# Performance work log

Measured on AMD Instinct MI355X. Metric: run time of the kernel, lower is better.

## Reference

```python
import jax, jax.numpy as jnp
import numpy as np

K = 32
D = 64
N_ITER = 10


def setup_inputs() -> dict:
    key = jax.random.key(0)
    k1, k2 = jax.random.split(key)
    B = 65536
    x = jax.random.normal(k1, (B, D), dtype=jnp.float32)
    c = jnp.zeros((K,), dtype=jnp.float32)
    mu = jax.random.normal(k2, (K, D), dtype=jnp.float32) * 0.1
    A = jnp.tile(jnp.eye(D, dtype=jnp.float32)[None], (K, 1, 1))
    alpha = jnp.float32(0.1)
    return {"x": x, "c": c, "mu": mu, "A": A, "alpha": alpha}


def _grad_phi(x, c, mu, A):
    # Precision matrices Sigma_i^{-1} = A_i^T A_i : (k, d, d)
    P = jnp.einsum('kji,kjl->kil', A, A)
    diff = x[:, None, :] - mu[None, :, :]          # (B, k, d)
    Pd = jnp.einsum('kij,bkj->bki', P, diff)       # Sigma^{-1} (x - mu)
    quad = jnp.einsum('bki,bki->bk', diff, Pd)     # (B, k)
    # Analytic gradient of phi(x) = logsumexp_i(c_i - 0.5 q_i):
    # grad = -sum_i softmax_i(c_i - 0.5 q_i) * Sigma_i^{-1}(x - mu_i)
    w = jax.nn.softmax(c[None, :] - 0.5 * quad, axis=1)  # (B, k)
    return -jnp.einsum('bk,bki->bi', w, Pd)


def reference(x, c, mu, A, alpha):
    def step(x_cur, _):
        x_new = x_cur + alpha * _grad_phi(x_cur, c, mu, A)
        return x_new, None
    x_final, _ = jax.lax.scan(step, x, None, length=N_ITER)
    return x_final
```

## Files before the change

### kernel.cpp

```cpp
#include <hip/hip_runtime.h>
#include <hip/hip_bf16.h>


typedef __attribute__((ext_vector_type(4))) float f32x4;
typedef __attribute__((ext_vector_type(8))) short bf16x8;

#define KC 32
#define NITER 10
#define XROW 72
#define WAVE_SCR 6656

static __device__ __forceinline__ unsigned pk_bf16(float a, float b) {
  __hip_bfloat16 ha = __float2bfloat16(a), hb = __float2bfloat16(b);
  unsigned short ua = *(unsigned short*)&ha, ub = *(unsigned short*)&hb;
  return (unsigned)ua | ((unsigned)ub << 16);
}

__global__ void precompute1(const float* __restrict__ A, const float* __restrict__ mu,
                            const float* __restrict__ c,
                            float* __restrict__ Pmu_g, float* __restrict__ e_g,
                            __hip_bfloat16* __restrict__ Psw) {
  __shared__ float Pk[64 * 64];
  __shared__ float Pmu_s[64];
  const int k = blockIdx.x, tid = threadIdx.x;
  const float* Ak = A + k * 4096;
  for (int idx = tid; idx < 4096; idx += 256) {
    int i = idx >> 6, l = idx & 63;
    float s = 0.f;
    for (int j = 0; j < 64; ++j) s += Ak[j * 64 + i] * Ak[j * 64 + l];
    Pk[idx] = s;
  }
  __syncthreads();
  if (tid < 64) {
    float s = 0.f;
    for (int l = 0; l < 64; ++l) s += Pk[tid * 64 + l] * mu[k * 64 + l];
    Pmu_s[tid] = s;
    Pmu_g[k * 64 + tid] = s;
  }
  __syncthreads();
  if (tid == 0) {
    float s = 0.f;
    for (int i = 0; i < 64; ++i) s += mu[k * 64 + i] * Pmu_s[i];
    e_g[k] = c[k] - 0.5f * s;
  }
  for (int idx = tid; idx < 4096; idx += 256) {
    int f = idx >> 9, lane = (idx >> 3) & 63, j = idx & 7;
    int mt = f >> 1, s = f & 1, qq = lane >> 4, l4 = lane & 15;
    float v = Pk[(s * 32 + qq * 8 + j) * 64 + mt * 16 + l4];
    Psw[k * 4096 + idx] = __float2bfloat16(v);
  }
}

__global__ void precompute2(const float* __restrict__ Pmu_g,
                            __hip_bfloat16* __restrict__ PmuA,
                            __hip_bfloat16* __restrict__ PmuB) {
  const int tid = threadIdx.x;
  for (int idx = tid; idx < 2048; idx += 256) {
    int f = idx >> 9, lane = (idx >> 3) & 63, j = idx & 7;
    int mtc = f >> 1, s = f & 1, qq = lane >> 4, l4 = lane & 15;
    PmuA[idx] = __float2bfloat16(Pmu_g[(mtc * 16 + l4) * 64 + s * 32 + qq * 8 + j]);
  }
  for (int idx = tid; idx < 2048; idx += 256) {
    int f = idx >> 9, lane = (idx >> 3) & 63, j = idx & 7;
    int qq = lane >> 4, l4 = lane & 15;
    PmuB[idx] = __float2bfloat16(Pmu_g[(qq * 8 + j) * 64 + f * 16 + l4]);
  }
}

__launch_bounds__(256, 2)
__global__ void denoise_main(const float* __restrict__ x_in,
                             const float* __restrict__ e_g,
                             const float* __restrict__ alpha_g,
                             const __hip_bfloat16* __restrict__ Psw,
                             const __hip_bfloat16* __restrict__ PmuA,
                             const __hip_bfloat16* __restrict__ PmuB,
                             float* __restrict__ out) {
  __shared__ __attribute__((aligned(16))) char scratch[4 * WAVE_SCR];

  const int tid = threadIdx.x;
  const int wave = tid >> 6, lane = tid & 63;
  const int q = lane >> 4, l4 = lane & 15;
  const int base_pt = blockIdx.x * 128 + wave * 32;
  const float alpha = alpha_g[0];

  char* sw = scratch + wave * WAVE_SCR;
  __hip_bfloat16* xsw = (__hip_bfloat16*)sw;
  float* pmxw = (float*)sw;
  __hip_bfloat16* wtw = (__hip_bfloat16*)(sw + 4608);

  const bf16x8* PswF = (const bf16x8*)Psw;
  const bf16x8* PmuAF = (const bf16x8*)PmuA;
  const bf16x8* PmuBF = (const bf16x8*)PmuB;

  float xm[4][2][4];
#pragma unroll
  for (int mt = 0; mt < 4; ++mt)
#pragma unroll
    for (int nt = 0; nt < 2; ++nt)
#pragma unroll
      for (int r = 0; r < 4; ++r)
        xm[mt][nt][r] = x_in[(base_pt + nt * 16 + l4) * 64 + mt * 16 + q * 4 + r];

  const f32x4 Z4 = {0.f, 0.f, 0.f, 0.f};

#pragma unroll 1
  for (int it = 0; it < NITER; ++it) {
#pragma unroll
    for (int mt = 0; mt < 4; ++mt)
#pragma unroll
      for (int nt = 0; nt < 2; ++nt) {
        unsigned u0 = pk_bf16(xm[mt][nt][0], xm[mt][nt][1]);
        unsigned u1 = pk_bf16(xm[mt][nt][2], xm[mt][nt][3]);
        uint2 v; v.x = u0; v.y = u1;
        *(uint2*)&xsw[(nt * 16 + l4) * XROW + mt * 16 + q * 4] = v;
      }

    bf16x8 bx[2][2];
#pragma unroll
    for (int s = 0; s < 2; ++s)
#pragma unroll
      for (int nt = 0; nt < 2; ++nt)
        bx[s][nt] = *(const bf16x8*)&xsw[(nt * 16 + l4) * XROW + s * 32 + q * 8];

    bf16x8 ap[2][4][2];
#pragma unroll
    for (int mt = 0; mt < 4; ++mt)
#pragma unroll
      for (int s = 0; s < 2; ++s)
        ap[0][mt][s] = PswF[(mt * 2 + s) * 64 + lane];

    f32x4 pmx[2][2];
#pragma unroll
    for (int mtc = 0; mtc < 2; ++mtc)
#pragma unroll
      for (int nt = 0; nt < 2; ++nt) {
        f32x4 acc = Z4;
#pragma unroll
        for (int s = 0; s < 2; ++s) {
          bf16x8 a = PmuAF[(mtc * 2 + s) * 64 + lane];
          acc = __builtin_amdgcn_mfma_f32_16x16x32_bf16(a, bx[s][nt], acc, 0, 0, 0);
        }
        pmx[mtc][nt] = acc;
      }
#pragma unroll
    for (int mtc = 0; mtc < 2; ++mtc)
#pragma unroll
      for (int nt = 0; nt < 2; ++nt)
#pragma unroll
        for (int r = 0; r < 4; ++r)
          pmxw[(mtc * 16 + q * 4 + r) * 32 + nt * 16 + l4] = pmx[mtc][nt][r];

    float accY[4][2][4];
#pragma unroll
    for (int mt = 0; mt < 4; ++mt)
#pragma unroll
      for (int nt = 0; nt < 2; ++nt)
#pragma unroll
        for (int r = 0; r < 4; ++r) accY[mt][nt][r] = 0.f;
    float lsum0 = 0.f, lsum1 = 0.f;

#pragma unroll 2
    for (int k = 0; k < KC; ++k) {
      const int cur = k & 1, nxt = cur ^ 1;
      const int kn = (k + 1) & (KC - 1);
#pragma unroll
      for (int mt = 0; mt < 4; ++mt)
#pragma unroll
        for (int s = 0; s < 2; ++s)
          ap[nxt][mt][s] = PswF[kn * 512 + (mt * 2 + s) * 64 + lane];

      f32x4 y[4][2];
#pragma unroll
      for (int mt = 0; mt < 4; ++mt)
#pragma unroll
        for (int nt = 0; nt < 2; ++nt) {
          f32x4 acc = Z4;
          acc = __builtin_amdgcn_mfma_f32_16x16x32_bf16(ap[cur][mt][0], bx[0][nt], acc, 0, 0, 0);
          acc = __builtin_amdgcn_mfma_f32_16x16x32_bf16(ap[cur][mt][1], bx[1][nt], acc, 0, 0, 0);
          y[mt][nt] = acc;
        }

      float xy0 = 0.f, xy1 = 0.f;
#pragma unroll
      for (int mt = 0; mt < 4; ++mt)
#pragma unroll
        for (int r = 0; r < 4; ++r) {
          xy0 += xm[mt][0][r] * y[mt][0][r];
          xy1 += xm[mt][1][r] * y[mt][1][r];
        }
      xy0 += __shfl_xor(xy0, 16, 64);
      xy0 += __shfl_xor(xy0, 32, 64);
      xy1 += __shfl_xor(xy1, 16, 64);
      xy1 += __shfl_xor(xy1, 32, 64);

      const float pk0 = pmxw[k * 32 + l4];
      const float pk1 = pmxw[k * 32 + 16 + l4];
      const float ek = e_g[k];
      const float w0 = __expf(ek + pk0 - 0.5f * xy0);
      const float w1 = __expf(ek + pk1 - 0.5f * xy1);
      lsum0 += w0;
      lsum1 += w1;
      if (q == 0) {
        wtw[l4 * 32 + k] = __float2bfloat16(w0);
        wtw[(16 + l4) * 32 + k] = __float2bfloat16(w1);
      }
#pragma unroll
      for (int mt = 0; mt < 4; ++mt)
#pragma unroll
        for (int r = 0; r < 4; ++r) {
          accY[mt][0][r] += w0 * y[mt][0][r];
          accY[mt][1][r] += w1 * y[mt][1][r];
        }
    }

    bf16x8 wtf[2];
#pragma unroll
    for (int nt = 0; nt < 2; ++nt)
      wtf[nt] = *(const bf16x8*)&wtw[(nt * 16 + l4) * 32 + q * 8];
    f32x4 pacc[4][2];
#pragma unroll
    for (int mt = 0; mt < 4; ++mt) {
      bf16x8 a = PmuBF[mt * 64 + lane];
      pacc[mt][0] = __builtin_amdgcn_mfma_f32_16x16x32_bf16(a, wtf[0], Z4, 0, 0, 0);
      pacc[mt][1] = __builtin_amdgcn_mfma_f32_16x16x32_bf16(a, wtf[1], Z4, 0, 0, 0);
    }

    const float c0 = alpha / lsum0;
    const float c1 = alpha / lsum1;
#pragma unroll
    for (int mt = 0; mt < 4; ++mt)
#pragma unroll
      for (int r = 0; r < 4; ++r) {
        xm[mt][0][r] += c0 * (pacc[mt][0][r] - accY[mt][0][r]);
        xm[mt][1][r] += c1 * (pacc[mt][1][r] - accY[mt][1][r]);
      }
  }

  float* outs = (float*)sw;
#pragma unroll
  for (int p = 0; p < 2; ++p) {
#pragma unroll
    for (int mt2 = 0; mt2 < 2; ++mt2)
#pragma unroll
      for (int nt = 0; nt < 2; ++nt)
#pragma unroll
        for (int r = 0; r < 4; ++r)
          outs[(nt * 16 + l4) * 32 + mt2 * 16 + q * 4 + r] = xm[p * 2 + mt2][nt][r];
#pragma unroll
    for (int rep = 0; rep < 16; ++rep) {
      int flat = rep * 64 + lane;
      int pt = flat >> 5, dp = flat & 31;
      out[(base_pt + pt) * 64 + p * 32 + dp] = outs[pt * 32 + dp];
    }
  }
}

extern "C" void kernel_launch(void* const* d_in, const int* in_sizes, int n_in,
                              void* d_out, int out_size, void* d_ws, size_t ws_size,
                              hipStream_t stream) {
  (void)in_sizes; (void)n_in; (void)out_size; (void)ws_size;
  const float* x = (const float*)d_in[0];
  const float* c = (const float*)d_in[1];
  const float* mu = (const float*)d_in[2];
  const float* A = (const float*)d_in[3];
  const float* alpha = (const float*)d_in[4];
  float* out = (float*)d_out;

  char* ws = (char*)d_ws;
  float* Pmu_g = (float*)(ws);
  float* e_g = (float*)(ws + 8192);
  __hip_bfloat16* PmuA = (__hip_bfloat16*)(ws + 8448);
  __hip_bfloat16* PmuB = (__hip_bfloat16*)(ws + 12544);
  __hip_bfloat16* Psw = (__hip_bfloat16*)(ws + 16640);

  precompute1<<<32, 256, 0, stream>>>(A, mu, c, Pmu_g, e_g, Psw);
  precompute2<<<1, 256, 0, stream>>>(Pmu_g, PmuA, PmuB);
  denoise_main<<<512, 256, 0, stream>>>(x, e_g, alpha, Psw, PmuA, PmuB, out);
}
```

Before: 306.2 us.

## Split component loop across wave pairs and reduce partial sums through LDS

Each pair of waves now shares 32 points, with each wave handling half of the 32 mixture components. The partial weighted sums and softmax denominators are exchanged through shared memory with block barriers. The grid doubles to 1024 blocks, which gives more waves to hide latency and halves the serial component loop per wave, at the cost of barriers, LDS traffic and a larger shared footprint. Other changes: cross-lane reductions now use ds_swizzle and permlane32 swap, the bias term is folded into the stored Pmu, stores are vectorized, and precompute1 gets an LDS-tiled A^T A.

```diff
diff --git a/kernel.cpp b/kernel.cpp
--- a/kernel.cpp
+++ b/kernel.cpp
@@ -6,9 +6,13 @@
 typedef __attribute__((ext_vector_type(8))) short bf16x8;
 
 #define KC 32
+#define KH 16
 #define NITER 10
 #define XROW 72
-#define WAVE_SCR 6656
+#define PW_BYTES 8704
+#define WT_PITCH 40
+#define WT_BYTES 2560
+#define LS_BYTES 256
 
 static __device__ __forceinline__ unsigned pk_bf16(float a, float b) {
   __hip_bfloat16 ha = __float2bfloat16(a), hb = __float2bfloat16(b);
@@ -16,38 +20,63 @@
   return (unsigned)ua | ((unsigned)ub << 16);
 }
 
+static __device__ __forceinline__ float red16(float x) {
+  int v = __builtin_amdgcn_ds_swizzle(__float_as_int(x), 0x401F);
+  return x + __int_as_float(v);
+}
+static __device__ __forceinline__ float red32(float x) {
+  int xi = __float_as_int(x);
+  auto pr = __builtin_amdgcn_permlane32_swap(xi, xi, false, false);
+  return __int_as_float(pr[0]) + __int_as_float(pr[1]);
+}
+
 __global__ void precompute1(const float* __restrict__ A, const float* __restrict__ mu,
                             const float* __restrict__ c,
                             float* __restrict__ Pmu_g, float* __restrict__ e_g,
                             __hip_bfloat16* __restrict__ Psw) {
+  __shared__ float As[64 * 64];
   __shared__ float Pk[64 * 64];
-  __shared__ float Pmu_s[64];
   const int k = blockIdx.x, tid = threadIdx.x;
   const float* Ak = A + k * 4096;
-  for (int idx = tid; idx < 4096; idx += 256) {
-    int i = idx >> 6, l = idx & 63;
-    float s = 0.f;
-    for (int j = 0; j < 64; ++j) s += Ak[j * 64 + i] * Ak[j * 64 + l];
-    Pk[idx] = s;
-  }
+  for (int idx = tid; idx < 1024; idx += 256)
+    *(f32x4*)&As[idx * 4] = *(const f32x4*)&Ak[idx * 4];
   __syncthreads();
+
+  const int i = tid >> 2, lg = tid & 3;
+  float acc[16] = {};
+  for (int j = 0; j < 64; ++j) {
+    float ai = As[j * 64 + i];
+    const f32x4* row = (const f32x4*)&As[j * 64 + lg * 16];
+#pragma unroll
+    for (int g = 0; g < 4; ++g) {
+      f32x4 v = row[g];
+#pragma unroll
+      for (int r = 0; r < 4; ++r) acc[g * 4 + r] += ai * v[r];
+    }
+  }
+#pragma unroll
+  for (int g = 0; g < 4; ++g)
+#pragma unroll
+    for (int r = 0; r < 4; ++r) Pk[i * 64 + lg * 16 + g * 4 + r] = acc[g * 4 + r];
+  __syncthreads();
+
   if (tid < 64) {
     float s = 0.f;
-    for (int l = 0; l < 64; ++l) s += Pk[tid * 64 + l] * mu[k * 64 + l];
-    Pmu_s[tid] = s;
+    for (int l = 0; l < 64; ++l) s += Pk[l * 64 + tid] * mu[k * 64 + l];
     Pmu_g[k * 64 + tid] = s;
-  }
-  __syncthreads();
-  if (tid == 0) {
-    float s = 0.f;
-    for (int i = 0; i < 64; ++i) s += mu[k * 64 + i] * Pmu_s[i];
-    e_g[k] = c[k] - 0.5f * s;
-  }
-  for (int idx = tid; idx < 4096; idx += 256) {
-    int f = idx >> 9, lane = (idx >> 3) & 63, j = idx & 7;
-    int mt = f >> 1, s = f & 1, qq = lane >> 4, l4 = lane & 15;
-    float v = Pk[(s * 32 + qq * 8 + j) * 64 + mt * 16 + l4];
-    Psw[k * 4096 + idx] = __float2bfloat16(v);
+    float v = mu[k * 64 + tid] * s;
+#pragma unroll
+    for (int off = 1; off < 64; off <<= 1) v += __shfl_xor(v, off, 64);
+    if (tid == 0) e_g[k] = c[k] - 0.5f * v;
+  }
+
+  unsigned* Psw32 = (unsigned*)(Psw + k * 4096);
+  for (int idx2 = tid; idx2 < 2048; idx2 += 256) {
+    int idx = idx2 << 1;
+    int f = idx >> 9, ln = (idx >> 3) & 63, j = idx & 7;
+    int mt = f >> 1, s = f & 1, qq = ln >> 4, l4 = ln & 15;
+    int col = mt * 16 + l4, rb = s * 32 + qq * 8 + j;
+    Psw32[idx2] = pk_bf16(Pk[rb * 64 + col], Pk[(rb + 1) * 64 + col]);
   }
 }
 
@@ -75,31 +104,36 @@
                              const __hip_bfloat16* __restrict__ PmuA,
                              const __hip_bfloat16* __restrict__ PmuB,
                              float* __restrict__ out) {
-  __shared__ __attribute__((aligned(16))) char scratch[4 * WAVE_SCR];
+  __shared__ __attribute__((aligned(16))) char scratch[4 * PW_BYTES + 2 * WT_BYTES + 2 * LS_BYTES];
 
   const int tid = threadIdx.x;
   const int wave = tid >> 6, lane = tid & 63;
+  const int pair = wave >> 1, khalf = wave & 1;
   const int q = lane >> 4, l4 = lane & 15;
-  const int base_pt = blockIdx.x * 128 + wave * 32;
+  const int base_pt = blockIdx.x * 64 + pair * 32;
   const float alpha = alpha_g[0];
-
-  char* sw = scratch + wave * WAVE_SCR;
-  __hip_bfloat16* xsw = (__hip_bfloat16*)sw;
-  float* pmxw = (float*)sw;
-  __hip_bfloat16* wtw = (__hip_bfloat16*)(sw + 4608);
+  const int kbase = khalf * KH;
+
+  char* pw = scratch + wave * PW_BYTES;
+  __hip_bfloat16* xsw = (__hip_bfloat16*)pw;
+  float* pmxw = (float*)pw;
+  float* exw = (float*)pw;
+  const float* exw_p = (const float*)(scratch + (wave ^ 1) * PW_BYTES);
+  __hip_bfloat16* wtw = (__hip_bfloat16*)(scratch + 4 * PW_BYTES + pair * WT_BYTES);
+  float* lsw = (float*)(scratch + 4 * PW_BYTES + 2 * WT_BYTES + pair * LS_BYTES);
 
   const bf16x8* PswF = (const bf16x8*)Psw;
   const bf16x8* PmuAF = (const bf16x8*)PmuA;
   const bf16x8* PmuBF = (const bf16x8*)PmuB;
 
-  float xm[4][2][4];
+  f32x4 xm[4][2];
 #pragma unroll
   for (int mt = 0; mt < 4; ++mt)
 #pragma unroll
     for (int nt = 0; nt < 2; ++nt)
-#pragma unroll
-      for (int r = 0; r < 4; ++r)
-        xm[mt][nt][r] = x_in[(base_pt + nt * 16 + l4) * 64 + mt * 16 + q * 4 + r];
+      xm[mt][nt] = *(const f32x4*)&x_in[(base_pt + nt * 16 + l4) * 64 + mt * 16 + q * 4];
+
+  const f32x4 ev = *(const f32x4*)&e_g[kbase + q * 4];
 
   const f32x4 Z4 = {0.f, 0.f, 0.f, 0.f};
 
@@ -109,9 +143,9 @@
     for (int mt = 0; mt < 4; ++mt)
 #pragma unroll
       for (int nt = 0; nt < 2; ++nt) {
-        unsigned u0 = pk_bf16(xm[mt][nt][0], xm[mt][nt][1]);
-        unsigned u1 = pk_bf16(xm[mt][nt][2], xm[mt][nt][3]);
-        uint2 v; v.x = u0; v.y = u1;
+        uint2 v;
+        v.x = pk_bf16(xm[mt][nt][0], xm[mt][nt][1]);
+        v.y = pk_bf16(xm[mt][nt][2], xm[mt][nt][3]);
         *(uint2*)&xsw[(nt * 16 + l4) * XROW + mt * 16 + q * 4] = v;
       }
 
@@ -127,42 +161,36 @@
     for (int mt = 0; mt < 4; ++mt)
 #pragma unroll
       for (int s = 0; s < 2; ++s)
-        ap[0][mt][s] = PswF[(mt * 2 + s) * 64 + lane];
-
-    f32x4 pmx[2][2];
-#pragma unroll
-    for (int mtc = 0; mtc < 2; ++mtc)
-#pragma unroll
-      for (int nt = 0; nt < 2; ++nt) {
-        f32x4 acc = Z4;
-#pragma unroll
-        for (int s = 0; s < 2; ++s) {
-          bf16x8 a = PmuAF[(mtc * 2 + s) * 64 + lane];
-          acc = __builtin_amdgcn_mfma_f32_16x16x32_bf16(a, bx[s][nt], acc, 0, 0, 0);
-        }
-        pmx[mtc][nt] = acc;
-      }
-#pragma unroll
-    for (int mtc = 0; mtc < 2; ++mtc)
-#pragma unroll
-      for (int nt = 0; nt < 2; ++nt)
-#pragma unroll
-        for (int r = 0; r < 4; ++r)
-          pmxw[(mtc * 16 + q * 4 + r) * 32 + nt * 16 + l4] = pmx[mtc][nt][r];
-
-    float accY[4][2][4];
-#pragma unroll
-    for (int mt = 0; mt < 4; ++mt)
-#pragma unroll
-      for (int nt = 0; nt < 2; ++nt)
-#pragma unroll
-        for (int r = 0; r < 4; ++r) accY[mt][nt][r] = 0.f;
+        ap[0][mt][s] = PswF[kbase * 512 + (mt * 2 + s) * 64 + lane];
+
+    f32x4 pmx[2];
+#pragma unroll
+    for (int nt = 0; nt < 2; ++nt) {
+      f32x4 acc = Z4;
+#pragma unroll
+      for (int s = 0; s < 2; ++s) {
+        bf16x8 a = PmuAF[(khalf * 2 + s) * 64 + lane];
+        acc = __builtin_amdgcn_mfma_f32_16x16x32_bf16(a, bx[s][nt], acc, 0, 0, 0);
+      }
+      pmx[nt] = acc;
+    }
+#pragma unroll
+    for (int nt = 0; nt < 2; ++nt)
+#pragma unroll
+      for (int r = 0; r < 4; ++r)
+        pmxw[(q * 4 + r) * 32 + nt * 16 + l4] = pmx[nt][r] + ev[r];
+
+    f32x4 accY[4][2];
+#pragma unroll
+    for (int mt = 0; mt < 4; ++mt)
+#pragma unroll
+      for (int nt = 0; nt < 2; ++nt) accY[mt][nt] = Z4;
     float lsum0 = 0.f, lsum1 = 0.f;
 
 #pragma unroll 2
-    for (int k = 0; k < KC; ++k) {
-      const int cur = k & 1, nxt = cur ^ 1;
-      const int kn = (k + 1) & (KC - 1);
+    for (int kk = 0; kk < KH; ++kk) {
+      const int cur = kk & 1, nxt = cur ^ 1;
+      const int kn = kbase + ((kk + 1) & (KH - 1));
 #pragma unroll
       for (int mt = 0; mt < 4; ++mt)
 #pragma unroll
@@ -180,43 +208,58 @@
           y[mt][nt] = acc;
         }
 
-      float xy0 = 0.f, xy1 = 0.f;
-#pragma unroll
-      for (int mt = 0; mt < 4; ++mt)
-#pragma unroll
-        for (int r = 0; r < 4; ++r) {
-          xy0 += xm[mt][0][r] * y[mt][0][r];
-          xy1 += xm[mt][1][r] * y[mt][1][r];
-        }
-      xy0 += __shfl_xor(xy0, 16, 64);
-      xy0 += __shfl_xor(xy0, 32, 64);
-      xy1 += __shfl_xor(xy1, 16, 64);
-      xy1 += __shfl_xor(xy1, 32, 64);
-
-      const float pk0 = pmxw[k * 32 + l4];
-      const float pk1 = pmxw[k * 32 + 16 + l4];
-      const float ek = e_g[k];
-      const float w0 = __expf(ek + pk0 - 0.5f * xy0);
-      const float w1 = __expf(ek + pk1 - 0.5f * xy1);
+      f32x4 d0 = xm[0][0] * y[0][0];
+      f32x4 d1 = xm[0][1] * y[0][1];
+#pragma unroll
+      for (int mt = 1; mt < 4; ++mt) {
+        d0 += xm[mt][0] * y[mt][0];
+        d1 += xm[mt][1] * y[mt][1];
+      }
+      float xy0 = (d0[0] + d0[1]) + (d0[2] + d0[3]);
+      float xy1 = (d1[0] + d1[1]) + (d1[2] + d1[3]);
+      xy0 = red32(red16(xy0));
+      xy1 = red32(red16(xy1));
+
+      const float pk0 = pmxw[kk * 32 + l4];
+      const float pk1 = pmxw[kk * 32 + 16 + l4];
+      const float w0 = __expf(pk0 - 0.5f * xy0);
+      const float w1 = __expf(pk1 - 0.5f * xy1);
       lsum0 += w0;
       lsum1 += w1;
       if (q == 0) {
-        wtw[l4 * 32 + k] = __float2bfloat16(w0);
-        wtw[(16 + l4) * 32 + k] = __float2bfloat16(w1);
-      }
-#pragma unroll
-      for (int mt = 0; mt < 4; ++mt)
-#pragma unroll
-        for (int r = 0; r < 4; ++r) {
-          accY[mt][0][r] += w0 * y[mt][0][r];
-          accY[mt][1][r] += w1 * y[mt][1][r];
-        }
-    }
+        wtw[l4 * WT_PITCH + kbase + kk] = __float2bfloat16(w0);
+        wtw[(16 + l4) * WT_PITCH + kbase + kk] = __float2bfloat16(w1);
+      }
+#pragma unroll
+      for (int mt = 0; mt < 4; ++mt) {
+        accY[mt][0] += w0 * y[mt][0];
+        accY[mt][1] += w1 * y[mt][1];
+      }
+    }
+
+#pragma unroll
+    for (int mt = 0; mt < 4; ++mt)
+#pragma unroll
+      for (int nt = 0; nt < 2; ++nt)
+        *(f32x4*)&exw[(nt * 16 + l4) * 68 + mt * 16 + q * 4] = accY[mt][nt];
+    if (q == 0) {
+      lsw[khalf * 32 + l4] = lsum0;
+      lsw[khalf * 32 + 16 + l4] = lsum1;
+    }
+    __syncthreads();
+
+#pragma unroll
+    for (int mt = 0; mt < 4; ++mt)
+#pragma unroll
+      for (int nt = 0; nt < 2; ++nt)
+        accY[mt][nt] += *(const f32x4*)&exw_p[(nt * 16 + l4) * 68 + mt * 16 + q * 4];
+    const float lt0 = lsum0 + lsw[(khalf ^ 1) * 32 + l4];
+    const float lt1 = lsum1 + lsw[(khalf ^ 1) * 32 + 16 + l4];
 
     bf16x8 wtf[2];
 #pragma unroll
     for (int nt = 0; nt < 2; ++nt)
-      wtf[nt] = *(const bf16x8*)&wtw[(nt * 16 + l4) * 32 + q * 8];
+      wtf[nt] = *(const bf16x8*)&wtw[(nt * 16 + l4) * WT_PITCH + q * 8];
     f32x4 pacc[4][2];
 #pragma unroll
     for (int mt = 0; mt < 4; ++mt) {
@@ -225,34 +268,22 @@
       pacc[mt][1] = __builtin_amdgcn_mfma_f32_16x16x32_bf16(a, wtf[1], Z4, 0, 0, 0);
     }
 
-    const float c0 = alpha / lsum0;
-    const float c1 = alpha / lsum1;
-#pragma unroll
-    for (int mt = 0; mt < 4; ++mt)
-#pragma unroll
-      for (int r = 0; r < 4; ++r) {
-        xm[mt][0][r] += c0 * (pacc[mt][0][r] - accY[mt][0][r]);
-        xm[mt][1][r] += c1 * (pacc[mt][1][r] - accY[mt][1][r]);
-      }
-  }
-
-  float* outs = (float*)sw;
-#pragma unroll
-  for (int p = 0; p < 2; ++p) {
-#pragma unroll
-    for (int mt2 = 0; mt2 < 2; ++mt2)
-#pragma unroll
-      for (int nt = 0; nt < 2; ++nt)
-#pragma unroll
-        for (int r = 0; r < 4; ++r)
-          outs[(nt * 16 + l4) * 32 + mt2 * 16 + q * 4 + r] = xm[p * 2 + mt2][nt][r];
-#pragma unroll
-    for (int rep = 0; rep < 16; ++rep) {
-      int flat = rep * 64 + lane;
-      int pt = flat >> 5, dp = flat & 31;
-      out[(base_pt + pt) * 64 + p * 32 + dp] = outs[pt * 32 + dp];
-    }
-  }
+    const float c0 = alpha / lt0;
+    const float c1 = alpha / lt1;
+#pragma unroll
+    for (int mt = 0; mt < 4; ++mt) {
+      xm[mt][0] += c0 * (pacc[mt][0] - accY[mt][0]);
+      xm[mt][1] += c1 * (pacc[mt][1] - accY[mt][1]);
+    }
+    __syncthreads();
+  }
+
+#pragma unroll
+  for (int mt2 = 0; mt2 < 2; ++mt2)
+#pragma unroll
+    for (int nt = 0; nt < 2; ++nt)
+      *(f32x4*)&out[(base_pt + nt * 16 + l4) * 64 + khalf * 32 + mt2 * 16 + q * 4] =
+          xm[khalf * 2 + mt2][nt];
 }
 
 extern "C" void kernel_launch(void* const* d_in, const int* in_sizes, int n_in,
@@ -275,5 +306,5 @@
 
   precompute1<<<32, 256, 0, stream>>>(A, mu, c, Pmu_g, e_g, Psw);
   precompute2<<<1, 256, 0, stream>>>(Pmu_g, PmuA, PmuB);
-  denoise_main<<<512, 256, 0, stream>>>(x, e_g, alpha, Psw, PmuA, PmuB, out);
-}
+  denoise_main<<<1024, 256, 0, stream>>>(x, e_g, alpha, Psw, PmuA, PmuB, out);
+}
```

Result: slower. 345.6 us (+12.9%).
